# Kernel optimization log

Measured on AMD Instinct MI355X. Metric: run time of the kernel, lower is better.

Reference implementation:

```python
import jax, jax.numpy as jnp
import numpy as np


def bilinear_sampler(img, flow):
    """Warp img (B,H,W,C) by per-pixel flow (B,H,W,2): sample at (x+u, y+v).
    Border handling: indices clipped to the image (edge padding)."""
    B, H, W, C = img.shape
    gy, gx = jnp.meshgrid(jnp.arange(H, dtype=img.dtype),
                          jnp.arange(W, dtype=img.dtype), indexing='ij')
    x = gx[None] + flow[..., 0]  # (B,H,W)
    y = gy[None] + flow[..., 1]
    x0f = jnp.floor(x)
    y0f = jnp.floor(y)
    wx = x - x0f  # fractional parts, differentiable w.r.t. flow
    wy = y - y0f
    x0 = jnp.clip(x0f.astype(jnp.int32), 0, W - 1)
    x1 = jnp.clip(x0f.astype(jnp.int32) + 1, 0, W - 1)
    y0 = jnp.clip(y0f.astype(jnp.int32), 0, H - 1)
    y1 = jnp.clip(y0f.astype(jnp.int32) + 1, 0, H - 1)
    b = jnp.arange(B)[:, None, None]
    Ia = img[b, y0, x0]  # (B,H,W,C)
    Ib = img[b, y1, x0]
    Ic = img[b, y0, x1]
    Id = img[b, y1, x1]
    wx = wx[..., None]
    wy = wy[..., None]
    return (Ia * (1 - wx) * (1 - wy) + Ib * (1 - wx) * wy
            + Ic * wx * (1 - wy) + Id * wx * wy)


def setup_inputs() -> dict:
    key = jax.random.key(0)
    k1, k2, k3, k4, k5, k6 = jax.random.split(key, 6)
    B, H, W = 8, 512, 512
    return {
        't': jax.random.uniform(k1, (B, 1, 1, 1), dtype=jnp.float32),
        'I0': jax.random.uniform(k2, (B, H, W, 3), dtype=jnp.float32),
        'I1': jax.random.uniform(k3, (B, H, W, 3), dtype=jnp.float32),
        'interp': jax.random.normal(k4, (B, H, W, 5), dtype=jnp.float32),
        'Fhat_t0': jax.random.normal(k5, (B, H, W, 2), dtype=jnp.float32),
        'Fhat_t1': jax.random.normal(k6, (B, H, W, 2), dtype=jnp.float32),
    }


def reference(t, I0, I1, interp, Fhat_t0, Fhat_t1):
    Ft0 = interp[..., 0:2] + Fhat_t0
    Ft1 = interp[..., 2:4] + Fhat_t1
    Vt0 = jax.nn.sigmoid(interp[..., 4:5])  # (B,H,W,1) -> broadcasts over RGB
    Vt1 = 1.0 - Vt0
    g0 = bilinear_sampler(I0, Ft0)
    g1 = bilinear_sampler(I1, Ft1)
    eps = 1e-12
    w0 = (1.0 - t) * Vt0
    w1 = t * Vt1
    It = (w0 * g0 + w1 * g1) / (w0 + w1 + eps)
    return It
```

## Files before the change

### kernel.cpp

```cpp
#include <hip/hip_runtime.h>
#include <hip/hip_fp16.h>

constexpr int B_ = 8;
constexpr int H_ = 512;
constexpr int W_ = 512;
constexpr int HW_ = H_ * W_;

constexpr int TS = 32;
constexpr int R_ = 4;
constexpr int RS = TS + 2 * R_;
constexpr int NSPX = RS * RS;


template <int IMG>
__device__ __forceinline__ void sampleT(const __half2* __restrict__ rgp,
                                        const __half2* __restrict__ bbp,
                                        const float* __restrict__ img,
                                        int gx0, int gy0,
                                        float sx, float sy, float g[3]) {
    float xf = floorf(sx), yf = floorf(sy);
    float wx = sx - xf, wy = sy - yf;
    int ix = (int)xf, iy = (int)yf;
    int x0 = min(max(ix, 0), W_ - 1);
    int x1 = min(max(ix + 1, 0), W_ - 1);
    int y0 = min(max(iy, 0), H_ - 1);
    int y1 = min(max(iy + 1, 0), H_ - 1);

    float w00 = (1.0f - wx) * (1.0f - wy);
    float w01 = wx * (1.0f - wy);
    float w10 = (1.0f - wx) * wy;
    float w11 = wx * wy;

    int lx0 = x0 - gx0, lx1 = x1 - gx0;
    int ly0 = y0 - gy0, ly1 = y1 - gy0;
    bool inT = ((unsigned)lx0 < (unsigned)RS) & ((unsigned)lx1 < (unsigned)RS) &
               ((unsigned)ly0 < (unsigned)RS) & ((unsigned)ly1 < (unsigned)RS);

    if (inT) {
        int p00 = ly0 * RS + lx0, p01 = ly0 * RS + lx1;
        int p10 = ly1 * RS + lx0, p11 = ly1 * RS + lx1;
        __half2 h00 = __float2half2_rn(w00);
        __half2 h01 = __float2half2_rn(w01);
        __half2 h10 = __float2half2_rn(w10);
        __half2 h11 = __float2half2_rn(w11);
        __half2 rg = __hmul2(h00, rgp[p00]);
        rg = __hfma2(h01, rgp[p01], rg);
        rg = __hfma2(h10, rgp[p10], rg);
        rg = __hfma2(h11, rgp[p11], rg);
        __half2 bb = __hmul2(h00, bbp[p00]);
        bb = __hfma2(h01, bbp[p01], bb);
        bb = __hfma2(h10, bbp[p10], bb);
        bb = __hfma2(h11, bbp[p11], bb);
        g[0] = __low2float(rg);
        g[1] = __high2float(rg);
        g[2] = (IMG == 0) ? __low2float(bb) : __high2float(bb);
    } else {
        const float* pa = img + ((size_t)y0 * W_ + x0) * 3;
        const float* pb = img + ((size_t)y0 * W_ + x1) * 3;
        const float* pc = img + ((size_t)y1 * W_ + x0) * 3;
        const float* pd = img + ((size_t)y1 * W_ + x1) * 3;
        #pragma unroll
        for (int ch = 0; ch < 3; ++ch)
            g[ch] = pa[ch] * w00 + pb[ch] * w01 +
                    pc[ch] * w10 + pd[ch] * w11;
    }
}

__global__ __launch_bounds__(256, 8) void frame_interp_tiled(
    const float* __restrict__ t,
    const float* __restrict__ I0,
    const float* __restrict__ I1,
    const float* __restrict__ interp,
    const float* __restrict__ F0,
    const float* __restrict__ F1,
    float* __restrict__ out)
{
    __shared__ __half2 lds_rg[2][NSPX];
    __shared__ __half2 lds_bb[NSPX];

    int tid = threadIdx.x;
    int bid = blockIdx.x;
    int b    = bid & 7;
    int tile = bid >> 3;
    int ty   = tile >> 4;
    int tx   = tile & 15;
    int gx0 = tx * TS - R_;
    int gy0 = ty * TS - R_;

    const float* img0 = I0 + (size_t)b * HW_ * 3;
    const float* img1 = I1 + (size_t)b * HW_ * 3;

    float tb = t[b];

    constexpr int FULL = NSPX / 256;
    constexpr int TAIL = NSPX - FULL * 256;
    float c0[FULL][3], c1[FULL][3];
    #pragma unroll
    for (int k = 0; k < FULL; ++k) {
        int p = tid + k * 256;
        int ry = p / RS;
        int rx = p - ry * RS;
        int gy = min(max(gy0 + ry, 0), H_ - 1);
        int gx = min(max(gx0 + rx, 0), W_ - 1);
        size_t s = ((size_t)gy * W_ + gx) * 3;
        __builtin_memcpy(c0[k], img0 + s, 12);
        __builtin_memcpy(c1[k], img1 + s, 12);
    }
    #pragma unroll
    for (int k = 0; k < FULL; ++k) {
        int p = tid + k * 256;
        lds_rg[0][p] = __floats2half2_rn(c0[k][0], c0[k][1]);
        lds_rg[1][p] = __floats2half2_rn(c1[k][0], c1[k][1]);
        lds_bb[p]    = __floats2half2_rn(c0[k][2], c1[k][2]);
    }
    if (tid < TAIL) {
        int p = FULL * 256 + tid;
        int ry = p / RS;
        int rx = p - ry * RS;
        int gy = min(max(gy0 + ry, 0), H_ - 1);
        int gx = min(max(gx0 + rx, 0), W_ - 1);
        size_t s = ((size_t)gy * W_ + gx) * 3;
        float d0[3], d1[3];
        __builtin_memcpy(d0, img0 + s, 12);
        __builtin_memcpy(d1, img1 + s, 12);
        lds_rg[0][p] = __floats2half2_rn(d0[0], d0[1]);
        lds_rg[1][p] = __floats2half2_rn(d1[0], d1[1]);
        lds_bb[p]    = __floats2half2_rn(d0[2], d1[2]);
    }
    __syncthreads();

    #pragma unroll
    for (int k = 0; k < 4; ++k) {
        int p   = tid + k * 256;
        int row = p >> 5;
        int col = p & 31;
        int gx = tx * TS + col;
        int gy = ty * TS + row;
        int idx = b * HW_ + gy * W_ + gx;

        const float* ip = interp + (size_t)idx * 5;
        float i01[2], i23[2];
        __builtin_memcpy(i01, ip, 8);
        __builtin_memcpy(i23, ip + 2, 8);
        float i4 = ip[4];
        float2 f0 = *(const float2*)(F0 + (size_t)idx * 2);
        float2 f1 = *(const float2*)(F1 + (size_t)idx * 2);

        float ft0x = i01[0] + f0.x;
        float ft0y = i01[1] + f0.y;
        float ft1x = i23[0] + f1.x;
        float ft1y = i23[1] + f1.y;
        float vt0  = 1.0f / (1.0f + __expf(-i4));

        float g0[3], g1[3];
        sampleT<0>(lds_rg[0], lds_bb, img0, gx0, gy0,
                   (float)gx + ft0x, (float)gy + ft0y, g0);
        sampleT<1>(lds_rg[1], lds_bb, img1, gx0, gy0,
                   (float)gx + ft1x, (float)gy + ft1y, g1);

        float w0 = (1.0f - tb) * vt0;
        float w1 = tb * (1.0f - vt0);
        float inv = 1.0f / (w0 + w1 + 1e-12f);

        float o[3];
        o[0] = (w0 * g0[0] + w1 * g1[0]) * inv;
        o[1] = (w0 * g0[1] + w1 * g1[1]) * inv;
        o[2] = (w0 * g0[2] + w1 * g1[2]) * inv;
        __builtin_memcpy(out + (size_t)idx * 3, o, 12);
    }
}

extern "C" void kernel_launch(void* const* d_in, const int* in_sizes, int n_in,
                              void* d_out, int out_size, void* d_ws, size_t ws_size,
                              hipStream_t stream) {
    const float* t      = (const float*)d_in[0];
    const float* I0     = (const float*)d_in[1];
    const float* I1     = (const float*)d_in[2];
    const float* interp = (const float*)d_in[3];
    const float* F0     = (const float*)d_in[4];
    const float* F1     = (const float*)d_in[5];
    float* out = (float*)d_out;

    int blocks = B_ * (H_ / TS) * (W_ / TS);
    frame_interp_tiled<<<blocks, 256, 0, stream>>>(t, I0, I1, interp, F0, F1, out);
}
```

Measured before the change: 164.3 us.

## Hoist per-pixel loads before LDS fill and vectorize 4-pixel contiguous I/O

Each thread now handles 4 horizontally adjacent pixels, so the interp, flow and output accesses become wide 16-byte-aligned vector loads and stores instead of scattered 8- and 12-byte accesses. These per-pixel loads, plus the tail halo load, are issued before the LDS conversion and barrier, with a scheduling barrier, so their latency overlaps the tile staging. Launch bounds are relaxed from 8 to 4 waves per SIMD to make room for the extra live registers. This may lower occupancy, and the 4-wide layout changes which output pixels a wavefront covers.

```diff
diff --git a/kernel.cpp b/kernel.cpp
--- a/kernel.cpp
+++ b/kernel.cpp
@@ -66,7 +66,7 @@
     }
 }
 
-__global__ __launch_bounds__(256, 8) void frame_interp_tiled(
+__global__ __launch_bounds__(256, 4) void frame_interp_tiled(
     const float* __restrict__ t,
     const float* __restrict__ I0,
     const float* __restrict__ I1,
@@ -106,6 +106,35 @@
         __builtin_memcpy(c0[k], img0 + s, 12);
         __builtin_memcpy(c1[k], img1 + s, 12);
     }
+    float d0[3], d1[3];
+    bool tail = tid < TAIL;
+    int pt = FULL * 256 + tid;
+    if (tail) {
+        int ry = pt / RS;
+        int rx = pt - ry * RS;
+        int gy = min(max(gy0 + ry, 0), H_ - 1);
+        int gx = min(max(gx0 + rx, 0), W_ - 1);
+        size_t s = ((size_t)gy * W_ + gx) * 3;
+        __builtin_memcpy(d0, img0 + s, 12);
+        __builtin_memcpy(d1, img1 + s, 12);
+    }
+
+    int row  = tid >> 3;
+    int colb = (tid & 7) * 4;
+    int gy_o = ty * TS + row;
+    int gx_o = tx * TS + colb;
+    size_t idx0 = (size_t)b * HW_ + (size_t)gy_o * W_ + gx_o;
+
+    const float* ipp = (const float*)__builtin_assume_aligned(interp + idx0 * 5, 16);
+    const float* f0p = (const float*)__builtin_assume_aligned(F0 + idx0 * 2, 16);
+    const float* f1p = (const float*)__builtin_assume_aligned(F1 + idx0 * 2, 16);
+    float ii[20], f0v[8], f1v[8];
+    __builtin_memcpy(ii, ipp, 80);
+    __builtin_memcpy(f0v, f0p, 32);
+    __builtin_memcpy(f1v, f1p, 32);
+
+    __builtin_amdgcn_sched_barrier(0);
+
     #pragma unroll
     for (int k = 0; k < FULL; ++k) {
         int p = tid + k * 256;
@@ -113,61 +142,37 @@
         lds_rg[1][p] = __floats2half2_rn(c1[k][0], c1[k][1]);
         lds_bb[p]    = __floats2half2_rn(c0[k][2], c1[k][2]);
     }
-    if (tid < TAIL) {
-        int p = FULL * 256 + tid;
-        int ry = p / RS;
-        int rx = p - ry * RS;
-        int gy = min(max(gy0 + ry, 0), H_ - 1);
-        int gx = min(max(gx0 + rx, 0), W_ - 1);
-        size_t s = ((size_t)gy * W_ + gx) * 3;
-        float d0[3], d1[3];
-        __builtin_memcpy(d0, img0 + s, 12);
-        __builtin_memcpy(d1, img1 + s, 12);
-        lds_rg[0][p] = __floats2half2_rn(d0[0], d0[1]);
-        lds_rg[1][p] = __floats2half2_rn(d1[0], d1[1]);
-        lds_bb[p]    = __floats2half2_rn(d0[2], d1[2]);
+    if (tail) {
+        lds_rg[0][pt] = __floats2half2_rn(d0[0], d0[1]);
+        lds_rg[1][pt] = __floats2half2_rn(d1[0], d1[1]);
+        lds_bb[pt]    = __floats2half2_rn(d0[2], d1[2]);
     }
     __syncthreads();
 
+    float o[12];
     #pragma unroll
     for (int k = 0; k < 4; ++k) {
-        int p   = tid + k * 256;
-        int row = p >> 5;
-        int col = p & 31;
-        int gx = tx * TS + col;
-        int gy = ty * TS + row;
-        int idx = b * HW_ + gy * W_ + gx;
-
-        const float* ip = interp + (size_t)idx * 5;
-        float i01[2], i23[2];
-        __builtin_memcpy(i01, ip, 8);
-        __builtin_memcpy(i23, ip + 2, 8);
-        float i4 = ip[4];
-        float2 f0 = *(const float2*)(F0 + (size_t)idx * 2);
-        float2 f1 = *(const float2*)(F1 + (size_t)idx * 2);
-
-        float ft0x = i01[0] + f0.x;
-        float ft0y = i01[1] + f0.y;
-        float ft1x = i23[0] + f1.x;
-        float ft1y = i23[1] + f1.y;
-        float vt0  = 1.0f / (1.0f + __expf(-i4));
+        float fx = (float)(gx_o + k);
+        float fy = (float)gy_o;
+        float sx0 = fx + ii[k * 5 + 0] + f0v[k * 2 + 0];
+        float sy0 = fy + ii[k * 5 + 1] + f0v[k * 2 + 1];
+        float sx1 = fx + ii[k * 5 + 2] + f1v[k * 2 + 0];
+        float sy1 = fy + ii[k * 5 + 3] + f1v[k * 2 + 1];
+        float vt0 = 1.0f / (1.0f + __expf(-ii[k * 5 + 4]));
 
         float g0[3], g1[3];
-        sampleT<0>(lds_rg[0], lds_bb, img0, gx0, gy0,
-                   (float)gx + ft0x, (float)gy + ft0y, g0);
-        sampleT<1>(lds_rg[1], lds_bb, img1, gx0, gy0,
-                   (float)gx + ft1x, (float)gy + ft1y, g1);
+        sampleT<0>(lds_rg[0], lds_bb, img0, gx0, gy0, sx0, sy0, g0);
+        sampleT<1>(lds_rg[1], lds_bb, img1, gx0, gy0, sx1, sy1, g1);
 
         float w0 = (1.0f - tb) * vt0;
         float w1 = tb * (1.0f - vt0);
         float inv = 1.0f / (w0 + w1 + 1e-12f);
-
-        float o[3];
-        o[0] = (w0 * g0[0] + w1 * g1[0]) * inv;
-        o[1] = (w0 * g0[1] + w1 * g1[1]) * inv;
-        o[2] = (w0 * g0[2] + w1 * g1[2]) * inv;
-        __builtin_memcpy(out + (size_t)idx * 3, o, 12);
+        o[k * 3 + 0] = (w0 * g0[0] + w1 * g1[0]) * inv;
+        o[k * 3 + 1] = (w0 * g0[1] + w1 * g1[1]) * inv;
+        o[k * 3 + 2] = (w0 * g0[2] + w1 * g1[2]) * inv;
     }
+    float* op = (float*)__builtin_assume_aligned(out + idx0 * 3, 16);
+    __builtin_memcpy(op, o, 48);
 }
 
 extern "C" void kernel_launch(void* const* d_in, const int* in_sizes, int n_in,
```

After: 164.7 us. No clear change (+0.2%).
